# Kernel tuning notes

Measured on AMD Instinct MI355X. Metric: run time of the kernel, lower is better.

Reference implementation:

```python
import jax, jax.numpy as jnp
import numpy as np

N = 100000
E = 1250000
D = 64
POS_DIM = 3


def _linear_params(key, fan_in, fan_out, bias=True):
    k1, k2 = jax.random.split(key)
    bound = 1.0 / np.sqrt(fan_in)
    W = jax.random.uniform(k1, (fan_in, fan_out), minval=-bound, maxval=bound, dtype=jnp.float32)
    if bias:
        b = jax.random.uniform(k2, (fan_out,), minval=-bound, maxval=bound, dtype=jnp.float32)
        return W, b
    return W


def setup_inputs() -> dict:
    key = jax.random.key(0)
    ks = jax.random.split(key, 10)
    x = jax.random.normal(ks[0], (N, D), dtype=jnp.float32)
    pos = jax.random.normal(ks[1], (N, POS_DIM), dtype=jnp.float32)
    edge_index = jax.random.randint(ks[2], (2, E), 0, N, dtype=jnp.int64)
    W_in, b_in = _linear_params(ks[3], D, D)
    W_lin = _linear_params(ks[4], D, D, bias=False)
    W_src = _linear_params(ks[5], D, D, bias=False)
    W_dst = _linear_params(ks[6], D, D, bias=False)
    W_pos, b_pos = _linear_params(ks[7], POS_DIM, D)
    W_out, b_out = _linear_params(ks[8], D, D)
    return {"x": x, "pos": pos, "edge_index": edge_index,
            "W_in": W_in, "b_in": b_in, "W_lin": W_lin, "W_src": W_src,
            "W_dst": W_dst, "W_pos": W_pos, "b_pos": b_pos,
            "W_out": W_out, "b_out": b_out}


def reference(x, pos, edge_index, W_in, b_in, W_lin, W_src, W_dst, W_pos, b_pos, W_out, b_out):
    n = x.shape[0]
    src, dst = edge_index[0], edge_index[1]  # j, i (PyG source_to_target)
    # lin_in + relu
    h = jax.nn.relu(x @ W_in + b_in)  # [N, D]
    # PointTransformerConv projections
    x_lin = h @ W_lin      # value projection, gathered at src (x_j)
    a_src = h @ W_src      # alpha_j side
    a_dst = h @ W_dst      # alpha_i side
    # per-edge positional MLP on pos_i - pos_j
    delta = (pos[dst] - pos[src]) @ W_pos + b_pos  # [E, D]
    # per-edge attention logits, per channel
    alpha = a_dst[dst] - a_src[src] + delta  # [E, D]
    # segment softmax over destination node groups (PyG softmax, eps=1e-16)
    seg_max = jax.ops.segment_max(alpha, dst, num_segments=n)
    alpha = jnp.exp(alpha - seg_max[dst])
    seg_sum = jax.ops.segment_sum(alpha, dst, num_segments=n)
    alpha = alpha / (seg_sum[dst] + 1e-16)
    # weighted messages, scatter-add aggregate
    msg = alpha * (x_lin[src] + delta)  # [E, D]
    out = jax.ops.segment_sum(msg, dst, num_segments=n)  # [N, D]
    # lin_out + relu
    return jax.nn.relu(out @ W_out + b_out)
```

## Files before the change

### kernel.cpp

```cpp
#include <hip/hip_runtime.h>

#define NN 100000
#define NE 1250000
#define NWIN 782
#define GA 256
#define CHUNK ((NE + GA - 1) / GA)
#define CAP16 16
#define OVFCAP 131072
#define WEDCAP 40

typedef __attribute__((ext_vector_type(4))) float f32x4;
typedef __attribute__((ext_vector_type(8))) short s16x8;

__device__ __forceinline__ short bfb(float f) {
    union { float f; unsigned u; } c; c.f = f;
    unsigned u = c.u + 0x7fffu + ((c.u >> 16) & 1u);
    return (short)(u >> 16);
}
__device__ __forceinline__ void splitbf(float v, short& hi, short& lo) {
    hi = bfb(v);
    union { unsigned u; float f; } c; c.u = ((unsigned)(unsigned short)hi) << 16;
    lo = bfb(v - c.f);
}
__device__ __forceinline__ float lo2f(unsigned u) {
    union { unsigned u; float f; } c; c.u = u << 16; return c.f;
}
__device__ __forceinline__ float hi2f(unsigned u) {
    union { unsigned u; float f; } c; c.u = u & 0xffff0000u; return c.f;
}

__global__ __launch_bounds__(256) void k_prep(
    const float* __restrict__ Wi, const float* __restrict__ Wl,
    const float* __restrict__ Ws, const float* __restrict__ Wo,
    short* __restrict__ P, int* __restrict__ ovf_cnt)
{
    const int t = blockIdx.x * 256 + threadIdx.x;
    if (t == 0) *ovf_cnt = 0;
    if (t >= 2048) return;
    const int mat = t >> 9, rem = t & 511;
    const int lane = rem & 63, cfg = rem >> 6;
    const int kh = cfg >> 2, nt = cfg & 3;
    const int m = lane & 15, q = lane >> 4;
    const float* W = mat == 0 ? Wi : mat == 1 ? Wl : mat == 2 ? Ws : Wo;
    s16x8 v;
    #pragma unroll
    for (int i = 0; i < 8; ++i)
        v[i] = bfb(W[(kh * 32 + q * 8 + i) * 64 + nt * 16 + m]);
    *(s16x8*)&P[(size_t)t * 8] = v;
}

__global__ __launch_bounds__(256) void k_front(
    const int* __restrict__ ei, unsigned* __restrict__ stage, int* __restrict__ gcnt,
    int2* __restrict__ ovf, int* __restrict__ ovf_cnt,
    const float* __restrict__ x, const short* __restrict__ P,
    const float* __restrict__ b_in,
    const float* __restrict__ pos, const float* __restrict__ W_pos,
    unsigned* __restrict__ AXb)
{
    __shared__ int lcnt[NWIN];
    __shared__ float hT[4][16 * 68];

    if (blockIdx.x < GA) {
        const int g = blockIdx.x;
        for (int i = threadIdx.x; i < NWIN; i += 256) lcnt[i] = 0;
        __syncthreads();
        unsigned* myStage = stage + (size_t)g * NWIN * CAP16;
        const int e0 = g * CHUNK;
        const int e1 = (e0 + CHUNK < NE) ? e0 + CHUNK : NE;
        for (int e = e0 + threadIdx.x; e < e1; e += 256) {
            const int s = ei[e], d = ei[NE + e];
            const int b = d >> 7;
            const int c = atomicAdd(&lcnt[b], 1);
            if (c < CAP16) {
                myStage[b * CAP16 + c] = (unsigned)s | ((unsigned)(d & 127) << 17);
            } else {
                const int o = atomicAdd(ovf_cnt, 1);
                if (o < OVFCAP) ovf[o] = make_int2(s, d);
            }
        }
        __syncthreads();
        for (int i = threadIdx.x; i < NWIN; i += 256)
            gcnt[i * GA + g] = lcnt[i] < CAP16 ? lcnt[i] : CAP16;
        return;
    }

    const int lane = threadIdx.x & 63;
    const int wid  = threadIdx.x >> 6;
    const int m = lane & 15, q = lane >> 4;

    s16x8 Wf[3][2][4];
    #pragma unroll
    for (int mat = 0; mat < 3; ++mat)
        #pragma unroll
        for (int kh = 0; kh < 2; ++kh)
            #pragma unroll
            for (int nt = 0; nt < 4; ++nt)
                Wf[mat][kh][nt] = *(const s16x8*)&P[((size_t)mat * 512 + (kh * 4 + nt) * 64 + lane) * 8];
    float bin[4], wpv0[4], wpv1[4], wpv2[4];
    #pragma unroll
    for (int nt = 0; nt < 4; ++nt) {
        bin[nt]  = b_in[nt * 16 + m];
        wpv0[nt] = W_pos[nt * 16 + m];
        wpv1[nt] = W_pos[64 + nt * 16 + m];
        wpv2[nt] = W_pos[128 + nt * 16 + m];
    }

    const int wave = (blockIdx.x - GA) * 4 + wid, nw = (gridDim.x - GA) * 4;
    for (int chunk = wave; chunk < NN / 16; chunk += nw) {
        const int r0 = chunk * 16;
        const float* xr = x + (size_t)(r0 + m) * 64;
        float xv[16];
        *(float4*)&xv[0]  = *(const float4*)(xr + q * 8);
        *(float4*)&xv[4]  = *(const float4*)(xr + q * 8 + 4);
        *(float4*)&xv[8]  = *(const float4*)(xr + 32 + q * 8);
        *(float4*)&xv[12] = *(const float4*)(xr + 32 + q * 8 + 4);
        s16x8 ahi0, alo0, ahi1, alo1;
        #pragma unroll
        for (int i = 0; i < 8; ++i) {
            short h, l;
            splitbf(xv[i], h, l);     ahi0[i] = h; alo0[i] = l;
            splitbf(xv[8 + i], h, l); ahi1[i] = h; alo1[i] = l;
        }
        #pragma unroll
        for (int nt = 0; nt < 4; ++nt) {
            f32x4 acc = {0.f, 0.f, 0.f, 0.f};
            acc = __builtin_amdgcn_mfma_f32_16x16x32_bf16(alo0, Wf[0][0][nt], acc, 0, 0, 0);
            acc = __builtin_amdgcn_mfma_f32_16x16x32_bf16(alo1, Wf[0][1][nt], acc, 0, 0, 0);
            acc = __builtin_amdgcn_mfma_f32_16x16x32_bf16(ahi0, Wf[0][0][nt], acc, 0, 0, 0);
            acc = __builtin_amdgcn_mfma_f32_16x16x32_bf16(ahi1, Wf[0][1][nt], acc, 0, 0, 0);
            #pragma unroll
            for (int r = 0; r < 4; ++r) {
                float hv = acc[r] + bin[nt];
                hT[wid][(q * 4 + r) * 68 + nt * 16 + m] = hv > 0.f ? hv : 0.f;
            }
        }
        float hv[16];
        *(float4*)&hv[0]  = *(const float4*)&hT[wid][m * 68 + q * 8];
        *(float4*)&hv[4]  = *(const float4*)&hT[wid][m * 68 + q * 8 + 4];
        *(float4*)&hv[8]  = *(const float4*)&hT[wid][m * 68 + 32 + q * 8];
        *(float4*)&hv[12] = *(const float4*)&hT[wid][m * 68 + 32 + q * 8 + 4];
        s16x8 hhi0, hlo0, hhi1, hlo1;
        #pragma unroll
        for (int i = 0; i < 8; ++i) {
            short h, l;
            splitbf(hv[i], h, l);     hhi0[i] = h; hlo0[i] = l;
            splitbf(hv[8 + i], h, l); hhi1[i] = h; hlo1[i] = l;
        }
        float px[4], py[4], pz[4];
        #pragma unroll
        for (int r = 0; r < 4; ++r) {
            const float* pp = pos + (size_t)(r0 + q * 4 + r) * 3;
            px[r] = pp[0]; py[r] = pp[1]; pz[r] = pp[2];
        }
        #pragma unroll
        for (int nt = 0; nt < 4; ++nt) {
            f32x4 aS = {0.f, 0.f, 0.f, 0.f}, aL = {0.f, 0.f, 0.f, 0.f};
            aS = __builtin_amdgcn_mfma_f32_16x16x32_bf16(hlo0, Wf[2][0][nt], aS, 0, 0, 0);
            aS = __builtin_amdgcn_mfma_f32_16x16x32_bf16(hlo1, Wf[2][1][nt], aS, 0, 0, 0);
            aS = __builtin_amdgcn_mfma_f32_16x16x32_bf16(hhi0, Wf[2][0][nt], aS, 0, 0, 0);
            aS = __builtin_amdgcn_mfma_f32_16x16x32_bf16(hhi1, Wf[2][1][nt], aS, 0, 0, 0);
            aL = __builtin_amdgcn_mfma_f32_16x16x32_bf16(hlo0, Wf[1][0][nt], aL, 0, 0, 0);
            aL = __builtin_amdgcn_mfma_f32_16x16x32_bf16(hlo1, Wf[1][1][nt], aL, 0, 0, 0);
            aL = __builtin_amdgcn_mfma_f32_16x16x32_bf16(hhi0, Wf[1][0][nt], aL, 0, 0, 0);
            aL = __builtin_amdgcn_mfma_f32_16x16x32_bf16(hhi1, Wf[1][1][nt], aL, 0, 0, 0);
            #pragma unroll
            for (int r = 0; r < 4; ++r) {
                const float sp = fmaf(px[r], wpv0[nt], fmaf(py[r], wpv1[nt], pz[r] * wpv2[nt]));
                const unsigned p = (unsigned)(unsigned short)bfb(aS[r] + sp)
                                 | ((unsigned)(unsigned short)bfb(aL[r] - sp) << 16);
                AXb[(size_t)(r0 + q * 4 + r) * 64 + nt * 16 + m] = p;
            }
        }
    }
}

__global__ __launch_bounds__(256) void k_passB(
    const unsigned* __restrict__ stage, const int* __restrict__ gcnt,
    const int2* __restrict__ ovf, const int* __restrict__ ovf_cnt,
    int* __restrict__ slots, int* __restrict__ deg)
{
    __shared__ int slotsL[128 * WEDCAP];
    __shared__ int cntL[128];
    const int b = blockIdx.x;
    const int t = threadIdx.x;
    if (t < 128) cntL[t] = 0;
    __syncthreads();
    const int n = min(gcnt[b * GA + t], CAP16);
    const unsigned* cell = stage + (size_t)t * NWIN * CAP16 + b * CAP16;
    uint4 q0 = *(const uint4*)cell;
    uint4 q1 = *(const uint4*)(cell + 4);
    uint4 q2 = *(const uint4*)(cell + 8);
    uint4 q3 = *(const uint4*)(cell + 12);
    const unsigned eb[16] = {q0.x, q0.y, q0.z, q0.w, q1.x, q1.y, q1.z, q1.w,
                             q2.x, q2.y, q2.z, q2.w, q3.x, q3.y, q3.z, q3.w};
    #pragma unroll
    for (int i = 0; i < CAP16; ++i)
        if (i < n) {
            const int d7 = (int)(eb[i] >> 17);
            const int c = atomicAdd(&cntL[d7], 1);
            if (c < WEDCAP) slotsL[d7 * WEDCAP + c] = (int)(eb[i] & 0x1ffff);
        }
    const int no = min(*ovf_cnt, OVFCAP);
    for (int i = t; i < no; i += 256) {
        const int2 sd = ovf[i];
        if ((sd.y >> 7) == b) {
            const int d7 = sd.y & 127;
            const int c = atomicAdd(&cntL[d7], 1);
            if (c < WEDCAP) slotsL[d7 * WEDCAP + c] = sd.x;
        }
    }
    __syncthreads();
    int4* dstq = (int4*)(slots + (size_t)b * 128 * WEDCAP);
    const int4* srcq = (const int4*)slotsL;
    #pragma unroll
    for (int i = 0; i < 5; ++i) dstq[i * 256 + t] = srcq[i * 256 + t];
    if (t < 128) {
        const int d = (b << 7) + t;
        if (d < NN) deg[d] = cntL[t] < WEDCAP ? cntL[t] : WEDCAP;
    }
}

__global__ __launch_bounds__(256) void k_agg(
    const int* __restrict__ deg_arr, const int* __restrict__ slots,
    const float* __restrict__ pos,
    const float* __restrict__ W_pos, const float* __restrict__ b_pos,
    const unsigned* __restrict__ AXb, float* __restrict__ V)
{
    const int lane = threadIdx.x & 63;
    const int d = __builtin_amdgcn_readfirstlane((int)((blockIdx.x * 256 + threadIdx.x) >> 6));
    if (d >= NN) return;
    const float pd0 = pos[d * 3 + 0], pd1 = pos[d * 3 + 1], pd2 = pos[d * 3 + 2];
    const float dlb = fmaf(pd0, W_pos[lane],
                      fmaf(pd1, W_pos[64 + lane],
                      fmaf(pd2, W_pos[128 + lane], b_pos[lane])));

    int deg = deg_arr[d]; deg = deg < WEDCAP ? deg : WEDCAP;
    const int* srow = slots + (size_t)d * WEDCAP;

    float Sa = 0.f, Ua = 0.f;
    if (deg > 0) {
        int cs[4], ns[4];
        unsigned cax[4], nax[4];
        {
            const int4 qd = *(const int4*)srow;
            cs[0] = qd.x;
            cs[1] = (1 < deg) ? qd.y : qd.x;
            cs[2] = (2 < deg) ? qd.z : qd.x;
            cs[3] = (3 < deg) ? qd.w : qd.x;
            #pragma unroll
            for (int k = 0; k < 4; ++k)
                cax[k] = AXb[(size_t)cs[k] * 64 + lane];
        }
        for (int j = 0; j < deg; j += 8) {
            if (j + 4 < deg) {
                const int4 qd = *(const int4*)(srow + j + 4);
                ns[0] = qd.x;
                ns[1] = (j + 5 < deg) ? qd.y : qd.x;
                ns[2] = (j + 6 < deg) ? qd.z : qd.x;
                ns[3] = (j + 7 < deg) ? qd.w : qd.x;
                #pragma unroll
                for (int k = 0; k < 4; ++k)
                    nax[k] = AXb[(size_t)ns[k] * 64 + lane];
            }
            #pragma unroll
            for (int k = 0; k < 4; ++k) {
                float wv = __expf(dlb - lo2f(cax[k]));
                if (j + k >= deg) wv = 0.f;
                Sa += wv;
                Ua = fmaf(wv, hi2f(cax[k]) + dlb, Ua);
            }
            if (j + 8 < deg) {
                const int4 qd = *(const int4*)(srow + j + 8);
                cs[0] = qd.x;
                cs[1] = (j + 9  < deg) ? qd.y : qd.x;
                cs[2] = (j + 10 < deg) ? qd.z : qd.x;
                cs[3] = (j + 11 < deg) ? qd.w : qd.x;
                #pragma unroll
                for (int k = 0; k < 4; ++k)
                    cax[k] = AXb[(size_t)cs[k] * 64 + lane];
            }
            if (j + 4 < deg) {
                #pragma unroll
                for (int k = 0; k < 4; ++k) {
                    float wv = __expf(dlb - lo2f(nax[k]));
                    if (j + 4 + k >= deg) wv = 0.f;
                    Sa += wv;
                    Ua = fmaf(wv, hi2f(nax[k]) + dlb, Ua);
                }
            }
        }
    }
    V[(size_t)d * 64 + lane] = Ua / (Sa + 1e-16f);
}

__global__ __launch_bounds__(256) void k_node_out(
    const float* __restrict__ V, const short* __restrict__ P,
    const float* __restrict__ b_out, float* __restrict__ out)
{
    const int lane = threadIdx.x & 63;
    const int wid  = threadIdx.x >> 6;
    const int m = lane & 15, q = lane >> 4;

    s16x8 Wf[2][4];
    #pragma unroll
    for (int kh = 0; kh < 2; ++kh)
        #pragma unroll
        for (int nt = 0; nt < 4; ++nt)
            Wf[kh][nt] = *(const s16x8*)&P[((size_t)3 * 512 + (kh * 4 + nt) * 64 + lane) * 8];
    float bo[4];
    #pragma unroll
    for (int nt = 0; nt < 4; ++nt) bo[nt] = b_out[nt * 16 + m];

    const int wave = blockIdx.x * 4 + wid, nw = gridDim.x * 4;
    for (int chunk = wave; chunk < NN / 16; chunk += nw) {
        const int r0 = chunk * 16;
        const float* vr = V + (size_t)(r0 + m) * 64;
        float vv[16];
        *(float4*)&vv[0]  = *(const float4*)(vr + q * 8);
        *(float4*)&vv[4]  = *(const float4*)(vr + q * 8 + 4);
        *(float4*)&vv[8]  = *(const float4*)(vr + 32 + q * 8);
        *(float4*)&vv[12] = *(const float4*)(vr + 32 + q * 8 + 4);
        s16x8 ahi0, alo0, ahi1, alo1;
        #pragma unroll
        for (int i = 0; i < 8; ++i) {
            short h, l;
            splitbf(vv[i], h, l);     ahi0[i] = h; alo0[i] = l;
            splitbf(vv[8 + i], h, l); ahi1[i] = h; alo1[i] = l;
        }
        #pragma unroll
        for (int nt = 0; nt < 4; ++nt) {
            f32x4 acc = {0.f, 0.f, 0.f, 0.f};
            acc = __builtin_amdgcn_mfma_f32_16x16x32_bf16(alo0, Wf[0][nt], acc, 0, 0, 0);
            acc = __builtin_amdgcn_mfma_f32_16x16x32_bf16(alo1, Wf[1][nt], acc, 0, 0, 0);
            acc = __builtin_amdgcn_mfma_f32_16x16x32_bf16(ahi0, Wf[0][nt], acc, 0, 0, 0);
            acc = __builtin_amdgcn_mfma_f32_16x16x32_bf16(ahi1, Wf[1][nt], acc, 0, 0, 0);
            #pragma unroll
            for (int r = 0; r < 4; ++r) {
                float o = acc[r] + bo[nt];
                out[(size_t)(r0 + q * 4 + r) * 64 + nt * 16 + m] = o > 0.f ? o : 0.f;
            }
        }
    }
}

extern "C" void kernel_launch(void* const* d_in, const int* in_sizes, int n_in,
                              void* d_out, int out_size, void* d_ws, size_t ws_size,
                              hipStream_t stream) {
    const float* x     = (const float*)d_in[0];
    const float* pos   = (const float*)d_in[1];
    const int*   ei    = (const int*)d_in[2];
    const float* W_in  = (const float*)d_in[3];
    const float* b_in  = (const float*)d_in[4];
    const float* W_lin = (const float*)d_in[5];
    const float* W_src = (const float*)d_in[6];
    const float* W_pos = (const float*)d_in[8];
    const float* b_pos = (const float*)d_in[9];
    const float* W_out = (const float*)d_in[10];
    const float* b_out = (const float*)d_in[11];

    unsigned* AXb   = (unsigned*)d_ws;
    unsigned* stage = AXb + (size_t)NN * 64;
    int*      gcnt  = (int*)(stage + (size_t)GA * NWIN * CAP16);
    int*      slots = gcnt + (size_t)NWIN * GA;
    int*      deg   = slots + (size_t)NWIN * 128 * WEDCAP;
    float*    V     = (float*)(deg + NN);
    int2*     ovf   = (int2*)(V + (size_t)NN * 64);
    int*      ovfc  = (int*)(ovf + OVFCAP);
    short*    P     = (short*)(ovfc + 64);

    k_prep    <<<8,        256, 0, stream>>>(W_in, W_lin, W_src, W_out, P, ovfc);
    k_front   <<<GA + 512, 256, 0, stream>>>(ei, stage, gcnt, ovf, ovfc,
                                             x, P, b_in, pos, W_pos, AXb);
    k_passB   <<<NWIN,     256, 0, stream>>>(stage, gcnt, ovf, ovfc, slots, deg);
    k_agg     <<<(NN + 3) / 4, 256, 0, stream>>>(deg, slots, pos, W_pos, b_pos, AXb, V);
    k_node_out<<<512,      256, 0, stream>>>(V, P, b_out, (float*)d_out);
}
```

Before: 184.0 us.

## Precompute per-source exp weights so aggregation only sums gathered values

The softmax factor exp(dlb - s_j) is split into exp(dlb) times exp(-s_j). The per-source exponential and the exp-weighted value are computed once per node in the front kernel, and exp(dlb) cancels in the normalisation, so the per-edge loop in k_agg becomes plain additions with no exp. Padding slots now point to a zeroed sentinel row instead of duplicating the first neighbour, which removes the masking. In exchange, the max-subtraction stabilisation is gone, so large logits could overflow, and storing exp values in bf16 adds rounding error.

After: 186.9 us. About the same (+1.6%).

```diff
diff --git a/kernel.cpp b/kernel.cpp
--- a/kernel.cpp
+++ b/kernel.cpp
@@ -32,10 +32,12 @@
 __global__ __launch_bounds__(256) void k_prep(
     const float* __restrict__ Wi, const float* __restrict__ Wl,
     const float* __restrict__ Ws, const float* __restrict__ Wo,
-    short* __restrict__ P, int* __restrict__ ovf_cnt)
+    short* __restrict__ P, int* __restrict__ ovf_cnt,
+    unsigned* __restrict__ AXb)
 {
     const int t = blockIdx.x * 256 + threadIdx.x;
     if (t == 0) *ovf_cnt = 0;
+    if (t < 64) AXb[(size_t)NN * 64 + t] = 0u;
     if (t >= 2048) return;
     const int mat = t >> 9, rem = t & 511;
     const int lane = rem & 63, cfg = rem >> 6;
@@ -166,8 +168,10 @@
             #pragma unroll
             for (int r = 0; r < 4; ++r) {
                 const float sp = fmaf(px[r], wpv0[nt], fmaf(py[r], wpv1[nt], pz[r] * wpv2[nt]));
-                const unsigned p = (unsigned)(unsigned short)bfb(aS[r] + sp)
-                                 | ((unsigned)(unsigned short)bfb(aL[r] - sp) << 16);
+                const float ev = __expf(-(aS[r] + sp));
+                const float ex = ev * (aL[r] - sp);
+                const unsigned p = (unsigned)(unsigned short)bfb(ev)
+                                 | ((unsigned)(unsigned short)bfb(ex) << 16);
                 AXb[(size_t)(r0 + q * 4 + r) * 64 + nt * 16 + m] = p;
             }
         }
@@ -244,53 +248,50 @@
         {
             const int4 qd = *(const int4*)srow;
             cs[0] = qd.x;
-            cs[1] = (1 < deg) ? qd.y : qd.x;
-            cs[2] = (2 < deg) ? qd.z : qd.x;
-            cs[3] = (3 < deg) ? qd.w : qd.x;
+            cs[1] = (1 < deg) ? qd.y : NN;
+            cs[2] = (2 < deg) ? qd.z : NN;
+            cs[3] = (3 < deg) ? qd.w : NN;
             #pragma unroll
             for (int k = 0; k < 4; ++k)
-                cax[k] = AXb[(size_t)cs[k] * 64 + lane];
+                cax[k] = AXb[(unsigned)(cs[k] * 64 + lane)];
         }
         for (int j = 0; j < deg; j += 8) {
             if (j + 4 < deg) {
                 const int4 qd = *(const int4*)(srow + j + 4);
                 ns[0] = qd.x;
-                ns[1] = (j + 5 < deg) ? qd.y : qd.x;
-                ns[2] = (j + 6 < deg) ? qd.z : qd.x;
-                ns[3] = (j + 7 < deg) ? qd.w : qd.x;
+                ns[1] = (j + 5 < deg) ? qd.y : NN;
+                ns[2] = (j + 6 < deg) ? qd.z : NN;
+                ns[3] = (j + 7 < deg) ? qd.w : NN;
                 #pragma unroll
                 for (int k = 0; k < 4; ++k)
-                    nax[k] = AXb[(size_t)ns[k] * 64 + lane];
+                    nax[k] = AXb[(unsigned)(ns[k] * 64 + lane)];
             }
             #pragma unroll
             for (int k = 0; k < 4; ++k) {
-                float wv = __expf(dlb - lo2f(cax[k]));
-                if (j + k >= deg) wv = 0.f;
-                Sa += wv;
-                Ua = fmaf(wv, hi2f(cax[k]) + dlb, Ua);
+                Sa += lo2f(cax[k]);
+                Ua += hi2f(cax[k]);
             }
             if (j + 8 < deg) {
                 const int4 qd = *(const int4*)(srow + j + 8);
                 cs[0] = qd.x;
-                cs[1] = (j + 9  < deg) ? qd.y : qd.x;
-                cs[2] = (j + 10 < deg) ? qd.z : qd.x;
-                cs[3] = (j + 11 < deg) ? qd.w : qd.x;
+                cs[1] = (j + 9  < deg) ? qd.y : NN;
+                cs[2] = (j + 10 < deg) ? qd.z : NN;
+                cs[3] = (j + 11 < deg) ? qd.w : NN;
                 #pragma unroll
                 for (int k = 0; k < 4; ++k)
-                    cax[k] = AXb[(size_t)cs[k] * 64 + lane];
+                    cax[k] = AXb[(unsigned)(cs[k] * 64 + lane)];
             }
             if (j + 4 < deg) {
                 #pragma unroll
                 for (int k = 0; k < 4; ++k) {
-                    float wv = __expf(dlb - lo2f(nax[k]));
-                    if (j + 4 + k >= deg) wv = 0.f;
-                    Sa += wv;
-                    Ua = fmaf(wv, hi2f(nax[k]) + dlb, Ua);
+                    Sa += lo2f(nax[k]);
+                    Ua += hi2f(nax[k]);
                 }
             }
         }
     }
-    V[(size_t)d * 64 + lane] = Ua / (Sa + 1e-16f);
+    const float v = (deg > 0) ? Ua / (Sa + 1e-16f) + dlb : 0.f;
+    V[(size_t)d * 64 + lane] = v;
 }
 
 __global__ __launch_bounds__(256) void k_node_out(
@@ -359,7 +360,7 @@
     const float* b_out = (const float*)d_in[11];
 
     unsigned* AXb   = (unsigned*)d_ws;
-    unsigned* stage = AXb + (size_t)NN * 64;
+    unsigned* stage = AXb + (size_t)(NN + 1) * 64;
     int*      gcnt  = (int*)(stage + (size_t)GA * NWIN * CAP16);
     int*      slots = gcnt + (size_t)NWIN * GA;
     int*      deg   = slots + (size_t)NWIN * 128 * WEDCAP;
@@ -368,7 +369,7 @@
     int*      ovfc  = (int*)(ovf + OVFCAP);
     short*    P     = (short*)(ovfc + 64);
 
-    k_prep    <<<8,        256, 0, stream>>>(W_in, W_lin, W_src, W_out, P, ovfc);
+    k_prep    <<<8,        256, 0, stream>>>(W_in, W_lin, W_src, W_out, P, ovfc, AXb);
     k_front   <<<GA + 512, 256, 0, stream>>>(ei, stage, gcnt, ovf, ovfc,
                                              x, P, b_in, pos, W_pos, AXb);
     k_passB   <<<NWIN,     256, 0, stream>>>(stage, gcnt, ovf, ovfc, slots, deg);
```
